# Optimization experiments

Hardware: AMD Instinct MI355X
Metric: run time of the kernel (lower is better)

## Reference

```python
import jax, jax.numpy as jnp
import numpy as np

B, C, H, W = 8, 256, 64, 64


def setup_inputs() -> dict:
    key = jax.random.key(0)
    ks = jax.random.split(key, 9)
    s = 1.0 / np.sqrt(C)  # conv2d default init scale
    return {
        "foreground": jax.random.normal(ks[0], (B, C, H, W), jnp.float32),
        "background": jax.random.normal(ks[1], (B, C, H, W), jnp.float32),
        "mask": jax.random.uniform(ks[2], (B, C, H, W), jnp.float32),
        "Wq": jax.random.normal(ks[3], (C, C), jnp.float32) * s,
        "bq": jnp.zeros((C,), jnp.float32),
        "Wk": jax.random.normal(ks[4], (C, C), jnp.float32) * s,
        "bk": jnp.zeros((C,), jnp.float32),
        "Wv": jax.random.normal(ks[5], (C, C), jnp.float32) * s,
        "bv": jnp.zeros((C,), jnp.float32),
        "gamma": jnp.ones((1,), jnp.float32),
    }


def _conv1x1(x, Wt, b):
    # 1x1 conv == per-pixel channel matmul; x: [B,C,H,W], Wt: [Cout,Cin]
    return jnp.einsum('bchw,oc->bohw', x, Wt) + b[None, :, None, None]


def reference(foreground, background, mask, Wq, bq, Wk, bk, Wv, bv, gamma):
    b, c, h, w = foreground.shape
    hw = h * w
    # mask is already at feature resolution (interpolate would be identity)
    q = _conv1x1(foreground, Wq, bq).reshape(b, c, hw)   # [B,C,HW]
    k = _conv1x1(background, Wk, bk).reshape(b, c, hw)   # [B,C,HW]
    # bmm(q, k^T): channel-channel correlation [B,C,C]
    corr = jnp.einsum('bci,bdi->bcd', q, k)
    m_r = mask.reshape(b, c, hw)                          # [B,C,HW]
    # bmm(corr, m_r): mask-modulated scores [B,C,HW]
    scores = jnp.einsum('bcd,bdi->bci', corr, m_r)
    energy = jax.nn.softmax(scores, axis=-1)
    v = _conv1x1(foreground, Wv, bv).reshape(b, c, hw)
    attended = (energy * v).reshape(b, c, h, w)
    out = foreground * mask + gamma[0] * (1.0 - mask) * attended
    return out
```

## Files before the change

### kernel.cpp

```cpp
#include <hip/hip_runtime.h>
#include <math.h>

#define B_    8
#define C_    256
#define HW_   4096
#define CHW_  ((long)C_ * HW_)

#define BKT   32
#define LDH   40
#define KS    16
#define KCH   (HW_ / KS)

typedef __attribute__((ext_vector_type(8))) short bf16x8;
typedef __attribute__((ext_vector_type(4))) float f32x4;
#define MFMA_BF16(a, b, c) __builtin_amdgcn_mfma_f32_16x16x32_bf16((a), (b), (c), 0, 0, 0)

union frag_u { uint4 u4; bf16x8 bf; };

__device__ __forceinline__ void cvt_hl4(const float4 f, uint* h, uint* l) {
    uint u0 = __float_as_uint(f.x), u1 = __float_as_uint(f.y),
         u2 = __float_as_uint(f.z), u3 = __float_as_uint(f.w);
    uint h0 = (u0 + 0x8000u) & 0xFFFF0000u, h1 = (u1 + 0x8000u) & 0xFFFF0000u,
         h2 = (u2 + 0x8000u) & 0xFFFF0000u, h3 = (u3 + 0x8000u) & 0xFFFF0000u;
    h[0] = (h0 >> 16) | h1;
    h[1] = (h2 >> 16) | h3;
    float l0 = f.x - __uint_as_float(h0), l1 = f.y - __uint_as_float(h1),
          l2 = f.z - __uint_as_float(h2), l3 = f.w - __uint_as_float(h3);
    uint a0 = __float_as_uint(l0) & 0xFFFF0000u, a1 = __float_as_uint(l1) & 0xFFFF0000u,
         a2 = __float_as_uint(l2) & 0xFFFF0000u, a3 = __float_as_uint(l3) & 0xFFFF0000u;
    l[0] = (a0 >> 16) | a1;
    l[1] = (a2 >> 16) | a3;
}
__device__ __forceinline__ void cvt_h4(const float4 f, uint* h) {
    uint u0 = __float_as_uint(f.x), u1 = __float_as_uint(f.y),
         u2 = __float_as_uint(f.z), u3 = __float_as_uint(f.w);
    uint h0 = (u0 + 0x8000u) & 0xFFFF0000u, h1 = (u1 + 0x8000u) & 0xFFFF0000u,
         h2 = (u2 + 0x8000u) & 0xFFFF0000u, h3 = (u3 + 0x8000u) & 0xFFFF0000u;
    h[0] = (h0 >> 16) | h1;
    h[1] = (h2 >> 16) | h3;
}

__device__ __forceinline__ void cvt2_hl(float a, float b2, uint* h, uint* l) {
    uint ua = __float_as_uint(a), ub = __float_as_uint(b2);
    uint ha = (ua + 0x8000u) & 0xFFFF0000u, hb = (ub + 0x8000u) & 0xFFFF0000u;
    *h = (ha >> 16) | hb;
    float la = a - __uint_as_float(ha), lb = b2 - __uint_as_float(hb);
    *l = ((__float_as_uint(la) & 0xFFFF0000u) >> 16) | (__float_as_uint(lb) & 0xFFFF0000u);
}
__device__ __forceinline__ uint cvt2_h(float a, float b2) {
    uint ha = (__float_as_uint(a) + 0x8000u) & 0xFFFF0000u;
    uint hb = (__float_as_uint(b2) + 0x8000u) & 0xFFFF0000u;
    return (ha >> 16) | hb;
}

__global__ __launch_bounds__(256) void conv_w(
    const float* __restrict__ Wv, ushort* __restrict__ Wvh)
{
    const int i = (blockIdx.x * 256 + threadIdx.x) * 4;
    float4 v = *reinterpret_cast<const float4*>(&Wv[i]);
    uint h[2];
    cvt_h4(v, h);
    *reinterpret_cast<uint2*>(&Wvh[i]) = make_uint2(h[0], h[1]);
}

__global__ __launch_bounds__(256) void transpose_cvt(
    const float* __restrict__ mask, const float* __restrict__ fg,
    ushort* __restrict__ mTh, ushort* __restrict__ mTl, ushort* __restrict__ fTh)
{
    __shared__ float Ms[64][65];
    __shared__ float Fs[64][65];

    const int b  = blockIdx.z;
    const int c0 = blockIdx.y * 64;
    const int i0 = blockIdx.x * 64;
    const int t  = threadIdx.x;

    const int lr = t >> 2;
    const int lc = (t & 3) * 16;
    const float* mp = mask + (long)b * CHW_ + (long)(c0 + lr) * HW_ + i0 + lc;
    const float* fp = fg   + (long)b * CHW_ + (long)(c0 + lr) * HW_ + i0 + lc;
    #pragma unroll
    for (int j = 0; j < 16; j += 4) {
        *reinterpret_cast<float4*>(&Ms[lr][lc + j]) = *reinterpret_cast<const float4*>(mp + j);
        *reinterpret_cast<float4*>(&Fs[lr][lc + j]) = *reinterpret_cast<const float4*>(fp + j);
    }
    __syncthreads();

    const int oi = t >> 2;
    const int oc = (t & 3) * 16;
    uint hm[8], lm[8], hf[8];
    #pragma unroll
    for (int j = 0; j < 8; ++j) {
        const float m0v = Ms[oc + 2 * j][oi], m1v = Ms[oc + 2 * j + 1][oi];
        cvt2_hl(m0v, m1v, &hm[j], &lm[j]);
        hf[j] = cvt2_h(Fs[oc + 2 * j][oi], Fs[oc + 2 * j + 1][oi]);
    }
    const long ro = ((long)b * HW_ + i0 + oi) * C_ + c0 + oc;
    *reinterpret_cast<uint4*>(&mTh[ro])     = make_uint4(hm[0], hm[1], hm[2], hm[3]);
    *reinterpret_cast<uint4*>(&mTh[ro + 8]) = make_uint4(hm[4], hm[5], hm[6], hm[7]);
    *reinterpret_cast<uint4*>(&mTl[ro])     = make_uint4(lm[0], lm[1], lm[2], lm[3]);
    *reinterpret_cast<uint4*>(&mTl[ro + 8]) = make_uint4(lm[4], lm[5], lm[6], lm[7]);
    *reinterpret_cast<uint4*>(&fTh[ro])     = make_uint4(hf[0], hf[1], hf[2], hf[3]);
    *reinterpret_cast<uint4*>(&fTh[ro + 8]) = make_uint4(hf[4], hf[5], hf[6], hf[7]);
}

__global__ __launch_bounds__(256, 3) void gemm_nt_mfma(
    const float* __restrict__ F, const float* __restrict__ G,
    float* __restrict__ part,
    float* __restrict__ fsum, float* __restrict__ gsum)
{
    __shared__ ushort Ah[128 * LDH], Al[128 * LDH], Bh[128 * LDH], Bl[128 * LDH];

    const int z  = blockIdx.z;
    const int b  = z >> 4;
    const int ks = z & (KS - 1);
    const int c0 = blockIdx.y * 128;
    const int d0 = blockIdx.x * 128;
    const float* Fb = F + (long)b * CHW_ + (long)ks * KCH;
    const float* Gb = G + (long)b * CHW_ + (long)ks * KCH;
    const bool doF = (blockIdx.x == 0);
    const bool doG = (blockIdx.y == 0);

    const int t    = threadIdx.x;
    const int srow = t & 127;
    const int skf  = (t >> 7) * 16;
    const int lane = t & 63, w = t >> 6;
    const int col  = lane & 15, quad = lane >> 4;
    const int wm   = (w >> 1) * 64, wn = (w & 1) * 64;

    f32x4 acc[4][4] = {};
    float rsF = 0.0f, rsG = 0.0f;

    for (int kt = 0; kt < KCH; kt += BKT) {
        {
            const float* s = &Fb[(long)(c0 + srow) * HW_ + kt + skf];
            float4 v0 = *reinterpret_cast<const float4*>(s);
            float4 v1 = *reinterpret_cast<const float4*>(s + 4);
            float4 v2 = *reinterpret_cast<const float4*>(s + 8);
            float4 v3 = *reinterpret_cast<const float4*>(s + 12);
            if (doF) {
                rsF += (v0.x + v0.y + v0.z + v0.w) + (v1.x + v1.y + v1.z + v1.w)
                     + (v2.x + v2.y + v2.z + v2.w) + (v3.x + v3.y + v3.z + v3.w);
            }
            uint h[4], l[4];
            cvt_hl4(v0, h + 0, l + 0);
            cvt_hl4(v1, h + 2, l + 2);
            *reinterpret_cast<uint4*>(&Ah[srow * LDH + skf]) = make_uint4(h[0], h[1], h[2], h[3]);
            *reinterpret_cast<uint4*>(&Al[srow * LDH + skf]) = make_uint4(l[0], l[1], l[2], l[3]);
            cvt_hl4(v2, h + 0, l + 0);
            cvt_hl4(v3, h + 2, l + 2);
            *reinterpret_cast<uint4*>(&Ah[srow * LDH + skf + 8]) = make_uint4(h[0], h[1], h[2], h[3]);
            *reinterpret_cast<uint4*>(&Al[srow * LDH + skf + 8]) = make_uint4(l[0], l[1], l[2], l[3]);
        }
        {
            const float* s = &Gb[(long)(d0 + srow) * HW_ + kt + skf];
            float4 v0 = *reinterpret_cast<const float4*>(s);
            float4 v1 = *reinterpret_cast<const float4*>(s + 4);
            float4 v2 = *reinterpret_cast<const float4*>(s + 8);
            float4 v3 = *reinterpret_cast<const float4*>(s + 12);
            if (doG) {
                rsG += (v0.x + v0.y + v0.z + v0.w) + (v1.x + v1.y + v1.z + v1.w)
                     + (v2.x + v2.y + v2.z + v2.w) + (v3.x + v3.y + v3.z + v3.w);
            }
            uint h[4], l[4];
            cvt_hl4(v0, h + 0, l + 0);
            cvt_hl4(v1, h + 2, l + 2);
            *reinterpret_cast<uint4*>(&Bh[srow * LDH + skf]) = make_uint4(h[0], h[1], h[2], h[3]);
            *reinterpret_cast<uint4*>(&Bl[srow * LDH + skf]) = make_uint4(l[0], l[1], l[2], l[3]);
            cvt_hl4(v2, h + 0, l + 0);
            cvt_hl4(v3, h + 2, l + 2);
            *reinterpret_cast<uint4*>(&Bh[srow * LDH + skf + 8]) = make_uint4(h[0], h[1], h[2], h[3]);
            *reinterpret_cast<uint4*>(&Bl[srow * LDH + skf + 8]) = make_uint4(l[0], l[1], l[2], l[3]);
        }
        __syncthreads();

        bf16x8 bfh[4], bfl[4];
        #pragma unroll
        for (int tj = 0; tj < 4; ++tj) {
            const int r = (wn + tj * 16 + col) * LDH + quad * 8;
            bfh[tj] = *reinterpret_cast<const bf16x8*>(&Bh[r]);
            bfl[tj] = *reinterpret_cast<const bf16x8*>(&Bl[r]);
        }
        #pragma unroll
        for (int ti = 0; ti < 4; ++ti) {
            const int r = (wm + ti * 16 + col) * LDH + quad * 8;
            bf16x8 afh = *reinterpret_cast<const bf16x8*>(&Ah[r]);
            bf16x8 afl = *reinterpret_cast<const bf16x8*>(&Al[r]);
            #pragma unroll
            for (int tj = 0; tj < 4; ++tj) {
                acc[ti][tj] = MFMA_BF16(afh, bfh[tj], acc[ti][tj]);
                acc[ti][tj] = MFMA_BF16(afh, bfl[tj], acc[ti][tj]);
                acc[ti][tj] = MFMA_BF16(afl, bfh[tj], acc[ti][tj]);
            }
        }
        __syncthreads();
    }

    if (doF) atomicAdd(&fsum[b * C_ + c0 + srow], rsF);
    if (doG) atomicAdd(&gsum[b * C_ + d0 + srow], rsG);

    float* P = part + (long)z * C_ * C_;
    #pragma unroll
    for (int ti = 0; ti < 4; ++ti) {
        const int m = c0 + wm + ti * 16 + quad * 4;
        #pragma unroll
        for (int tj = 0; tj < 4; ++tj) {
            const int n = d0 + wn + tj * 16 + col;
            #pragma unroll
            for (int r = 0; r < 4; ++r)
                P[(long)(m + r) * C_ + n] = acc[ti][tj][r];
        }
    }
}

__global__ __launch_bounds__(256, 2) void gemm_stats_mfma(
    const ushort* __restrict__ corrh, const ushort* __restrict__ corrl,
    const ushort* __restrict__ mTh,   const ushort* __restrict__ mTl,
    float* __restrict__ pmax, float* __restrict__ psum)
{
    __shared__ float pm[2][128], ps[2][128];

    const int b  = blockIdx.z;
    const int m0 = blockIdx.y * 128;
    const int n0 = blockIdx.x * 128;
    const ushort* Ahb = corrh + (long)b * C_ * C_;
    const ushort* Alb = corrl + (long)b * C_ * C_;
    const ushort* Bhb = mTh + (long)b * HW_ * C_;
    const ushort* Blb = mTl + (long)b * HW_ * C_;

    const int t    = threadIdx.x;
    const int lane = t & 63, w = t >> 6;
    const int col  = lane & 15, quad = lane >> 4;
    const int wm   = (w >> 1) * 64, wn = (w & 1) * 64;

    f32x4 acc[4][4] = {};

    #pragma unroll 1
    for (int kt = 0; kt < C_; kt += BKT) {
        bf16x8 ah[4], al[4], bh[4], bl[4];
        #pragma unroll
        for (int ti = 0; ti < 4; ++ti) {
            const long oa = (long)(m0 + wm + ti * 16 + col) * C_ + kt + quad * 8;
            ah[ti] = *reinterpret_cast<const bf16x8*>(&Ahb[oa]);
            al[ti] = *reinterpret_cast<const bf16x8*>(&Alb[oa]);
        }
        #pragma unroll
        for (int tj = 0; tj < 4; ++tj) {
            const long ob = (long)(n0 + wn + tj * 16 + col) * C_ + kt + quad * 8;
            bh[tj] = *reinterpret_cast<const bf16x8*>(&Bhb[ob]);
            bl[tj] = *reinterpret_cast<const bf16x8*>(&Blb[ob]);
        }
        #pragma unroll
        for (int tj = 0; tj < 4; ++tj) {
            #pragma unroll
            for (int ti = 0; ti < 4; ++ti) {
                acc[ti][tj] = MFMA_BF16(ah[ti], bh[tj], acc[ti][tj]);
                acc[ti][tj] = MFMA_BF16(ah[ti], bl[tj], acc[ti][tj]);
                acc[ti][tj] = MFMA_BF16(al[ti], bh[tj], acc[ti][tj]);
            }
        }
    }

    #pragma unroll
    for (int ti = 0; ti < 4; ++ti) {
        #pragma unroll
        for (int r = 0; r < 4; ++r) {
            float mx = fmaxf(fmaxf(acc[ti][0][r], acc[ti][1][r]),
                             fmaxf(acc[ti][2][r], acc[ti][3][r]));
            mx = fmaxf(mx, __shfl_xor(mx, 1));
            mx = fmaxf(mx, __shfl_xor(mx, 2));
            mx = fmaxf(mx, __shfl_xor(mx, 4));
            mx = fmaxf(mx, __shfl_xor(mx, 8));
            float se2 = __expf(acc[ti][0][r] - mx) + __expf(acc[ti][1][r] - mx)
                      + __expf(acc[ti][2][r] - mx) + __expf(acc[ti][3][r] - mx);
            se2 += __shfl_xor(se2, 1);
            se2 += __shfl_xor(se2, 2);
            se2 += __shfl_xor(se2, 4);
            se2 += __shfl_xor(se2, 8);
            if (col == 0) {
                const int rb = wm + ti * 16 + quad * 4 + r;
                pm[w & 1][rb] = mx;
                ps[w & 1][rb] = se2;
            }
        }
    }
    __syncthreads();
    if (t < 128) {
        const float a0 = pm[0][t], a1 = pm[1][t];
        const float gm = fmaxf(a0, a1);
        const float gs = ps[0][t] * __expf(a0 - gm) + ps[1][t] * __expf(a1 - gm);
        const long rowg = (long)b * C_ + m0 + t;
        pmax[rowg * 32 + blockIdx.x] = gm;
        psum[rowg * 32 + blockIdx.x] = gs;
    }
}

__global__ __launch_bounds__(256, 2) void gemm_fused_final(
    const ushort* __restrict__ corrh, const ushort* __restrict__ corrl,
    const ushort* __restrict__ Wvh,
    const ushort* __restrict__ mTh,   const ushort* __restrict__ mTl,
    const ushort* __restrict__ fTh,
    const float* __restrict__ mask,   const float* __restrict__ fg,
    const float* __restrict__ pmax,   const float* __restrict__ psum,
    const float* __restrict__ bv,     const float* __restrict__ gamma,
    float* __restrict__ out)
{
    __shared__ float sm[128], si[128];

    const int b  = blockIdx.z;
    const int m0 = blockIdx.y * 128;
    const int n0 = blockIdx.x * 128;
    const ushort* Ahb = corrh + (long)b * C_ * C_;
    const ushort* Alb = corrl + (long)b * C_ * C_;
    const ushort* Bhb = mTh + (long)b * HW_ * C_;
    const ushort* Blb = mTl + (long)b * HW_ * C_;
    const ushort* Bfb = fTh + (long)b * HW_ * C_;

    const int t    = threadIdx.x;
    const int lane = t & 63, w = t >> 6;
    const int col  = lane & 15, quad = lane >> 4;
    const int wm   = (w >> 1) * 64, wn = (w & 1) * 64;

    if (t < 128) {
        const long rowg = (long)b * C_ + m0 + t;
        const float* pmr = pmax + rowg * 32;
        const float* psr = psum + rowg * 32;
        float gm = -INFINITY;
        #pragma unroll
        for (int i = 0; i < 32; ++i) gm = fmaxf(gm, pmr[i]);
        float gs = 0.0f;
        #pragma unroll
        for (int i = 0; i < 32; ++i) gs += psr[i] * __expf(pmr[i] - gm);
        sm[t] = gm;
        si[t] = 1.0f / gs;
    }

    f32x4 acc_s[4][4] = {};
    f32x4 acc_v[4][4] = {};

    #pragma unroll 1
    for (int kt = 0; kt < C_; kt += BKT) {
        bf16x8 ah[4], al[4], aw[4], bh[4], bl[4], bf[4];
        #pragma unroll
        for (int ti = 0; ti < 4; ++ti) {
            const long oa = (long)(m0 + wm + ti * 16 + col) * C_ + kt + quad * 8;
            ah[ti] = *reinterpret_cast<const bf16x8*>(&Ahb[oa]);
            al[ti] = *reinterpret_cast<const bf16x8*>(&Alb[oa]);
            aw[ti] = *reinterpret_cast<const bf16x8*>(&Wvh[oa]);
        }
        #pragma unroll
        for (int tj = 0; tj < 4; ++tj) {
            const long ob = (long)(n0 + wn + tj * 16 + col) * C_ + kt + quad * 8;
            bh[tj] = *reinterpret_cast<const bf16x8*>(&Bhb[ob]);
            bl[tj] = *reinterpret_cast<const bf16x8*>(&Blb[ob]);
            bf[tj] = *reinterpret_cast<const bf16x8*>(&Bfb[ob]);
        }
        #pragma unroll
        for (int tj = 0; tj < 4; ++tj) {
            #pragma unroll
            for (int ti = 0; ti < 4; ++ti) {
                acc_s[ti][tj] = MFMA_BF16(ah[ti], bh[tj], acc_s[ti][tj]);
                acc_s[ti][tj] = MFMA_BF16(ah[ti], bl[tj], acc_s[ti][tj]);
                acc_s[ti][tj] = MFMA_BF16(al[ti], bh[tj], acc_s[ti][tj]);
                acc_v[ti][tj] = MFMA_BF16(aw[ti], bf[tj], acc_v[ti][tj]);
            }
        }
    }

    __syncthreads();

    const float g = gamma[0];
    #pragma unroll
    for (int ti = 0; ti < 4; ++ti) {
        #pragma unroll
        for (int r = 0; r < 4; ++r) {
            const int lrow = wm + ti * 16 + quad * 4 + r;
            const float mx  = sm[lrow];
            const float inv = si[lrow] * g;
            #pragma unroll
            for (int tj = 0; tj < 4; ++tj)
                acc_s[ti][tj][r] = __expf(acc_s[ti][tj][r] - mx) * inv;
        }
    }

    #pragma unroll
    for (int ti = 0; ti < 4; ++ti) {
        const int m = m0 + wm + ti * 16 + quad * 4;
        #pragma unroll
        for (int r = 0; r < 4; ++r) {
            const float bvm = bv[m + r];
            #pragma unroll
            for (int tj = 0; tj < 4; ++tj) {
                const int n = n0 + wn + tj * 16 + col;
                const long e = (long)b * CHW_ + (long)(m + r) * HW_ + n;
                const float f  = fg[e];
                const float mk = mask[e];
                const float vv = acc_v[ti][tj][r] + bvm;
                out[e] = f * mk + (1.0f - mk) * acc_s[ti][tj][r] * vv;
            }
        }
    }
}

__global__ __launch_bounds__(256) void reduce_part(
    const float* __restrict__ part, float* __restrict__ S1)
{
    const long idx = (long)blockIdx.x * 256 + threadIdx.x;
    const int  b   = (int)(idx >> 16);
    const long e   = idx & 65535;
    const float* p = part + ((long)b * KS) * 65536 + e;
    float s = 0.0f;
    #pragma unroll
    for (int ks = 0; ks < KS; ++ks) s += p[(long)ks * 65536];
    S1[idx] = s;
}

#define BK64 16
#define LDT64 68
__global__ __launch_bounds__(256) void gemm_nt64(
    const float* __restrict__ S1, const float* __restrict__ Wk,
    float* __restrict__ T)
{
    __shared__ float As[BK64][LDT64];
    __shared__ float Bs[BK64][LDT64];
    const int r0 = blockIdx.y * 64;
    const int d0 = blockIdx.x * 64;
    const int t   = threadIdx.x;
    const int tx  = t & 15, ty = t >> 4;
    const int tx4 = tx * 4, ty4 = ty * 4;
    const int am  = t >> 2, ak4 = (t & 3) * 4;

    float acc[4][4] = {};
    for (int k0 = 0; k0 < C_; k0 += BK64) {
        float4 av = *reinterpret_cast<const float4*>(&S1[(long)(r0 + am) * C_ + k0 + ak4]);
        float4 bw = *reinterpret_cast<const float4*>(&Wk[(long)(d0 + am) * C_ + k0 + ak4]);
        As[ak4+0][am]=av.x; As[ak4+1][am]=av.y; As[ak4+2][am]=av.z; As[ak4+3][am]=av.w;
        Bs[ak4+0][am]=bw.x; Bs[ak4+1][am]=bw.y; Bs[ak4+2][am]=bw.z; Bs[ak4+3][am]=bw.w;
        __syncthreads();
        #pragma unroll
        for (int kk = 0; kk < BK64; ++kk) {
            float4 a = *reinterpret_cast<const float4*>(&As[kk][ty4]);
            float4 x = *reinterpret_cast<const float4*>(&Bs[kk][tx4]);
            const float ar[4] = {a.x,a.y,a.z,a.w};
            const float xr[4] = {x.x,x.y,x.z,x.w};
            #pragma unroll
            for (int r = 0; r < 4; ++r)
                #pragma unroll
                for (int s = 0; s < 4; ++s)
                    acc[r][s] = fmaf(ar[r], xr[s], acc[r][s]);
        }
        __syncthreads();
    }
    #pragma unroll
    for (int r = 0; r < 4; ++r) {
        float4 o; o.x=acc[r][0]; o.y=acc[r][1]; o.z=acc[r][2]; o.w=acc[r][3];
        *reinterpret_cast<float4*>(&T[(long)(r0 + ty4 + r) * C_ + d0 + tx4]) = o;
    }
}

__global__ __launch_bounds__(256) void gemm_nn64_rank1(
    const float* __restrict__ Wq, const float* __restrict__ T,
    const float* __restrict__ Wk, const float* __restrict__ bk,
    const float* __restrict__ bq,
    const float* __restrict__ fsum, const float* __restrict__ gsum,
    ushort* __restrict__ corrh, ushort* __restrict__ corrl)
{
    __shared__ float As[BK64][LDT64];
    __shared__ float Bs[BK64][LDT64];
    __shared__ float u_s[64], wh_s[64];
    const int b  = blockIdx.z;
    const int m0 = blockIdx.y * 64;
    const int n0 = blockIdx.x * 64;
    const float* Tb = T + (long)b * C_ * C_;

    const int t   = threadIdx.x;
    const int tx  = t & 15, ty = t >> 4;
    const int tx4 = tx * 4, ty4 = ty * 4;
    const int am  = t >> 2, ak4 = (t & 3) * 4;
    const int xk  = ty,     xn4 = tx4;

    if (t < 64) {
        const float* wrow = Wq + (long)(m0 + t) * C_;
        const float* s = fsum + b * C_;
        float a = 0.0f;
        for (int e2 = 0; e2 < C_; ++e2) a = fmaf(wrow[e2], s[e2], a);
        u_s[t] = a;
    } else if (t < 128) {
        const int d = n0 + (t - 64);
        const float* wrow = Wk + (long)d * C_;
        const float* s = gsum + b * C_;
        float a = 0.0f;
        for (int e2 = 0; e2 < C_; ++e2) a = fmaf(wrow[e2], s[e2], a);
        wh_s[t - 64] = a + (float)HW_ * bk[d];
    }

    float acc[4][4] = {};
    for (int k0 = 0; k0 < C_; k0 += BK64) {
        float4 av = *reinterpret_cast<const float4*>(&Wq[(long)(m0 + am) * C_ + k0 + ak4]);
        float4 xv = *reinterpret_cast<const float4*>(&Tb[(long)(k0 + xk) * C_ + n0 + xn4]);
        As[ak4+0][am]=av.x; As[ak4+1][am]=av.y; As[ak4+2][am]=av.z; As[ak4+3][am]=av.w;
        *reinterpret_cast<float4*>(&Bs[xk][xn4]) = xv;
        __syncthreads();
        #pragma unroll
        for (int kk = 0; kk < BK64; ++kk) {
            float4 a = *reinterpret_cast<const float4*>(&As[kk][ty4]);
            float4 x = *reinterpret_cast<const float4*>(&Bs[kk][tx4]);
            const float ar[4] = {a.x,a.y,a.z,a.w};
            const float xr[4] = {x.x,x.y,x.z,x.w};
            #pragma unroll
            for (int r = 0; r < 4; ++r)
                #pragma unroll
                for (int s = 0; s < 4; ++s)
                    acc[r][s] = fmaf(ar[r], xr[s], acc[r][s]);
        }
        __syncthreads();
    }

    float4 bkv = *reinterpret_cast<const float4*>(&bk[n0 + tx4]);
    float4 whv = make_float4(wh_s[tx4], wh_s[tx4+1], wh_s[tx4+2], wh_s[tx4+3]);
    #pragma unroll
    for (int r = 0; r < 4; ++r) {
        const int m = m0 + ty4 + r;
        const float um = u_s[ty4 + r];
        const float bm = bq[m];
        float4 o;
        o.x = acc[r][0] + um*bkv.x + bm*whv.x;
        o.y = acc[r][1] + um*bkv.y + bm*whv.y;
        o.z = acc[r][2] + um*bkv.z + bm*whv.z;
        o.w = acc[r][3] + um*bkv.w + bm*whv.w;
        uint h[2], l[2];
        cvt_hl4(o, h, l);
        const long e = (long)b * C_ * C_ + (long)m * C_ + n0 + tx4;
        *reinterpret_cast<uint2*>(&corrh[e]) = make_uint2(h[0], h[1]);
        *reinterpret_cast<uint2*>(&corrl[e]) = make_uint2(l[0], l[1]);
    }
}

extern "C" void kernel_launch(void* const* d_in, const int* in_sizes, int n_in,
                              void* d_out, int out_size, void* d_ws, size_t ws_size,
                              hipStream_t stream)
{
    const float* fg    = (const float*)d_in[0];
    const float* bg    = (const float*)d_in[1];
    const float* mask  = (const float*)d_in[2];
    const float* Wq    = (const float*)d_in[3];
    const float* bq    = (const float*)d_in[4];
    const float* Wk    = (const float*)d_in[5];
    const float* bk    = (const float*)d_in[6];
    const float* Wv    = (const float*)d_in[7];
    const float* bv    = (const float*)d_in[8];
    const float* gamma = (const float*)d_in[9];
    float* out = (float*)d_out;

    char* ws = (char*)d_ws;
    float*  part   = (float*)(ws);
    float*  S1     = (float*)(ws + 33554432);
    float*  T      = (float*)(ws + 35651584);
    ushort* corrh  = (ushort*)(ws + 37748736);
    ushort* corrl  = (ushort*)(ws + 38797312);
    ushort* Wvh    = (ushort*)(ws + 39845888);
    float*  fsum   = (float*)(ws + 39976960);
    float*  gsum   = (float*)(ws + 39985152);
    float*  pmax   = (float*)(ws + 39993344);
    float*  psum   = (float*)(ws + 40255488);
    ushort* mTh    = (ushort*)(ws);
    ushort* mTl    = (ushort*)(ws + 16777216);
    ushort* fTh    = (ushort*)(ws + 40517632);

    const dim3 blk(256);

    hipMemsetAsync(fsum, 0, 16384, stream);

    conv_w<<<dim3(64), blk, 0, stream>>>(Wv, Wvh);

    gemm_nt_mfma<<<dim3(2, 2, B_ * KS), blk, 0, stream>>>(fg, bg, part, fsum, gsum);
    reduce_part<<<dim3(B_ * C_ * C_ / 256), blk, 0, stream>>>(part, S1);

    transpose_cvt<<<dim3(HW_ / 64, C_ / 64, B_), blk, 0, stream>>>(
        mask, fg, mTh, mTl, fTh);

    gemm_nt64<<<dim3(C_ / 64, B_ * C_ / 64), blk, 0, stream>>>(S1, Wk, T);
    gemm_nn64_rank1<<<dim3(4, 4, B_), blk, 0, stream>>>(
        Wq, T, Wk, bk, bq, fsum, gsum, corrh, corrl);

    gemm_stats_mfma<<<dim3(HW_ / 128, C_ / 128, B_), blk, 0, stream>>>(
        corrh, corrl, mTh, mTl, pmax, psum);

    gemm_fused_final<<<dim3(HW_ / 128, C_ / 128, B_), blk, 0, stream>>>(
        corrh, corrl, Wvh, mTh, mTl, fTh, mask, fg, pmax, psum, bv, gamma, out);
}
```

Measured before the change: 324.7 us.

## Double-buffer B operand tiles in LDS via async global_load_lds in both GEMMs

In the two mask GEMM kernels, the B-operand tiles (mask transpose hi/lo and the foreground bf16 tile) are now staged into shared memory with async global-to-LDS loads. The LDS layout is XOR-swizzled and double-buffered so the next k-chunk loads while the current one feeds MFMA. This is meant to cut redundant global reads, since B was previously loaded per wave and both M-waves read the same rows, and to hide load latency. The cost is more LDS use, a barrier every k-step, and a change of launch bounds to 3 blocks per CU for the stats kernel, which may add register pressure.

```diff
diff --git a/kernel.cpp b/kernel.cpp
--- a/kernel.cpp
+++ b/kernel.cpp
@@ -10,12 +10,18 @@
 #define LDH   40
 #define KS    16
 #define KCH   (HW_ / KS)
+#define NCH   (C_ / BKT)
 
 typedef __attribute__((ext_vector_type(8))) short bf16x8;
 typedef __attribute__((ext_vector_type(4))) float f32x4;
 #define MFMA_BF16(a, b, c) __builtin_amdgcn_mfma_f32_16x16x32_bf16((a), (b), (c), 0, 0, 0)
 
 union frag_u { uint4 u4; bf16x8 bf; };
+
+#define GLOAD_LDS16(src, dst)                                              \
+    __builtin_amdgcn_global_load_lds(                                      \
+        (const __attribute__((address_space(1))) void*)(src),              \
+        (__attribute__((address_space(3))) void*)(dst), 16, 0, 0)
 
 __device__ __forceinline__ void cvt_hl4(const float4 f, uint* h, uint* l) {
     uint u0 = __float_as_uint(f.x), u1 = __float_as_uint(f.y),
@@ -213,11 +219,12 @@
     }
 }
 
-__global__ __launch_bounds__(256, 2) void gemm_stats_mfma(
+__global__ __launch_bounds__(256, 3) void gemm_stats_mfma(
     const ushort* __restrict__ corrh, const ushort* __restrict__ corrl,
     const ushort* __restrict__ mTh,   const ushort* __restrict__ mTl,
     float* __restrict__ pmax, float* __restrict__ psum)
 {
+    __shared__ __align__(16) ushort Bst[2][2][4096];
     __shared__ float pm[2][128], ps[2][128];
 
     const int b  = blockIdx.z;
@@ -232,24 +239,59 @@
     const int lane = t & 63, w = t >> 6;
     const int col  = lane & 15, quad = lane >> 4;
     const int wm   = (w >> 1) * 64, wn = (w & 1) * 64;
+    const int qsw  = (lane & 3) ^ ((lane >> 3) & 3);
+    const int srw  = lane >> 2;
+
+    const ushort* gsrcs[2] = { Bhb, Blb };
+
+#define STAGE_S(buf, kk) do {                                              \
+    _Pragma("unroll")                                                      \
+    for (int a = 0; a < 2; ++a) {                                          \
+        _Pragma("unroll")                                                  \
+        for (int gg = 0; gg < 2; ++gg) {                                   \
+            const int g = w * 2 + gg;                                      \
+            const ushort* src = gsrcs[a]                                   \
+                + (long)(n0 + g * 16 + srw) * C_ + (kk) + qsw * 8;         \
+            GLOAD_LDS16(src, &Bst[buf][a][g * 512]);                       \
+        }                                                                  \
+    }                                                                      \
+} while (0)
+
+    int boff[4];
+    #pragma unroll
+    for (int tj = 0; tj < 4; ++tj) {
+        const int rowB = wn + tj * 16 + col;
+        boff[tj] = rowB * 64 + ((quad ^ ((rowB >> 1) & 3)) << 4);
+    }
 
     f32x4 acc[4][4] = {};
 
+    STAGE_S(0, 0);
+    __syncthreads();
+
+    int cur = 0;
     #pragma unroll 1
-    for (int kt = 0; kt < C_; kt += BKT) {
-        bf16x8 ah[4], al[4], bh[4], bl[4];
+    for (int kc = 0; kc < NCH; ++kc) {
+        const int kt = kc * BKT;
+
+        bf16x8 ah[4], al[4];
         #pragma unroll
         for (int ti = 0; ti < 4; ++ti) {
             const long oa = (long)(m0 + wm + ti * 16 + col) * C_ + kt + quad * 8;
             ah[ti] = *reinterpret_cast<const bf16x8*>(&Ahb[oa]);
             al[ti] = *reinterpret_cast<const bf16x8*>(&Alb[oa]);
         }
+
+        if (kc + 1 < NCH) STAGE_S(cur ^ 1, kt + BKT);
+
+        const char* base = (const char*)&Bst[cur][0][0];
+        bf16x8 bh[4], bl[4];
         #pragma unroll
         for (int tj = 0; tj < 4; ++tj) {
-            const long ob = (long)(n0 + wn + tj * 16 + col) * C_ + kt + quad * 8;
-            bh[tj] = *reinterpret_cast<const bf16x8*>(&Bhb[ob]);
-            bl[tj] = *reinterpret_cast<const bf16x8*>(&Blb[ob]);
-        }
+            bh[tj] = *reinterpret_cast<const bf16x8*>(base + boff[tj]);
+            bl[tj] = *reinterpret_cast<const bf16x8*>(base + 8192 + boff[tj]);
+        }
+
         #pragma unroll
         for (int tj = 0; tj < 4; ++tj) {
             #pragma unroll
@@ -259,7 +301,10 @@
                 acc[ti][tj] = MFMA_BF16(al[ti], bh[tj], acc[ti][tj]);
             }
         }
-    }
+        __syncthreads();
+        cur ^= 1;
+    }
+#undef STAGE_S
 
     #pragma unroll
     for (int ti = 0; ti < 4; ++ti) {
@@ -305,6 +350,7 @@
     const float* __restrict__ bv,     const float* __restrict__ gamma,
     float* __restrict__ out)
 {
+    __shared__ __align__(16) ushort Bst[2][3][4096];
     __shared__ float sm[128], si[128];
 
     const int b  = blockIdx.z;
@@ -320,6 +366,23 @@
     const int lane = t & 63, w = t >> 6;
     const int col  = lane & 15, quad = lane >> 4;
     const int wm   = (w >> 1) * 64, wn = (w & 1) * 64;
+    const int qsw  = (lane & 3) ^ ((lane >> 3) & 3);
+    const int srw  = lane >> 2;
+
+    const ushort* gsrcs[3] = { Bhb, Blb, Bfb };
+
+#define STAGE_F(buf, kk) do {                                              \
+    _Pragma("unroll")                                                      \
+    for (int a = 0; a < 3; ++a) {                                          \
+        _Pragma("unroll")                                                  \
+        for (int gg = 0; gg < 2; ++gg) {                                   \
+            const int g = w * 2 + gg;                                      \
+            const ushort* src = gsrcs[a]                                   \
+                + (long)(n0 + g * 16 + srw) * C_ + (kk) + qsw * 8;         \
+            GLOAD_LDS16(src, &Bst[buf][a][g * 512]);                       \
+        }                                                                  \
+    }                                                                      \
+} while (0)
 
     if (t < 128) {
         const long rowg = (long)b * C_ + m0 + t;
@@ -335,12 +398,25 @@
         si[t] = 1.0f / gs;
     }
 
+    int boff[4];
+    #pragma unroll
+    for (int tj = 0; tj < 4; ++tj) {
+        const int rowB = wn + tj * 16 + col;
+        boff[tj] = rowB * 64 + ((quad ^ ((rowB >> 1) & 3)) << 4);
+    }
+
     f32x4 acc_s[4][4] = {};
     f32x4 acc_v[4][4] = {};
 
+    STAGE_F(0, 0);
+    __syncthreads();
+
+    int cur = 0;
     #pragma unroll 1
-    for (int kt = 0; kt < C_; kt += BKT) {
-        bf16x8 ah[4], al[4], aw[4], bh[4], bl[4], bf[4];
+    for (int kc = 0; kc < NCH; ++kc) {
+        const int kt = kc * BKT;
+
+        bf16x8 ah[4], al[4], aw[4];
         #pragma unroll
         for (int ti = 0; ti < 4; ++ti) {
             const long oa = (long)(m0 + wm + ti * 16 + col) * C_ + kt + quad * 8;
@@ -348,13 +424,18 @@
             al[ti] = *reinterpret_cast<const bf16x8*>(&Alb[oa]);
             aw[ti] = *reinterpret_cast<const bf16x8*>(&Wvh[oa]);
         }
+
+        if (kc + 1 < NCH) STAGE_F(cur ^ 1, kt + BKT);
+
+        const char* base = (const char*)&Bst[cur][0][0];
+        bf16x8 bh[4], bl[4], bf[4];
         #pragma unroll
         for (int tj = 0; tj < 4; ++tj) {
-            const long ob = (long)(n0 + wn + tj * 16 + col) * C_ + kt + quad * 8;
-            bh[tj] = *reinterpret_cast<const bf16x8*>(&Bhb[ob]);
-            bl[tj] = *reinterpret_cast<const bf16x8*>(&Blb[ob]);
-            bf[tj] = *reinterpret_cast<const bf16x8*>(&Bfb[ob]);
-        }
+            bh[tj] = *reinterpret_cast<const bf16x8*>(base + boff[tj]);
+            bl[tj] = *reinterpret_cast<const bf16x8*>(base + 8192 + boff[tj]);
+            bf[tj] = *reinterpret_cast<const bf16x8*>(base + 16384 + boff[tj]);
+        }
+
         #pragma unroll
         for (int tj = 0; tj < 4; ++tj) {
             #pragma unroll
@@ -365,9 +446,10 @@
                 acc_v[ti][tj] = MFMA_BF16(aw[ti], bf[tj], acc_v[ti][tj]);
             }
         }
-    }
-
-    __syncthreads();
+        __syncthreads();
+        cur ^= 1;
+    }
+#undef STAGE_F
 
     const float g = gamma[0];
     #pragma unroll
```

After: 297.8 us. 1.09x faster.

## Stage MFMA operands through swizzled LDS via global_load_lds and coalesce stores

Applied to the files above, without the earlier changes.

The stats and fused-final GEMMs now stream their bf16 operand tiles into XOR-swizzled shared memory with direct global-to-LDS loads, instead of having each wave issue its own strided global vector loads. Occupancy hints go from 2 to 3 blocks. The split-K partial GEMM stages its output through LDS so it can write coalesced float4 rows, and reduce_part is vectorised to float4. The partial-max/sum buffers move to the S1 region and are read with float4 loads. In exchange this adds barrier overhead per K chunk, has no double buffering, and relies on the aliased workspace regions not overlapping any live data.

```diff
diff --git a/kernel.cpp b/kernel.cpp
--- a/kernel.cpp
+++ b/kernel.cpp
@@ -10,12 +10,19 @@
 #define LDH   40
 #define KS    16
 #define KCH   (HW_ / KS)
+#define NCH   (C_ / BKT)
+#define NPB   32
 
 typedef __attribute__((ext_vector_type(8))) short bf16x8;
 typedef __attribute__((ext_vector_type(4))) float f32x4;
 #define MFMA_BF16(a, b, c) __builtin_amdgcn_mfma_f32_16x16x32_bf16((a), (b), (c), 0, 0, 0)
 
 union frag_u { uint4 u4; bf16x8 bf; };
+
+#define GLOAD_LDS16(src, dst)                                              \
+    __builtin_amdgcn_global_load_lds(                                      \
+        (const __attribute__((address_space(1))) void*)(src),              \
+        (__attribute__((address_space(3))) void*)(dst), 16, 0, 0)
 
 __device__ __forceinline__ void cvt_hl4(const float4 f, uint* h, uint* l) {
     uint u0 = __float_as_uint(f.x), u1 = __float_as_uint(f.y),
@@ -109,7 +116,9 @@
     float* __restrict__ part,
     float* __restrict__ fsum, float* __restrict__ gsum)
 {
-    __shared__ ushort Ah[128 * LDH], Al[128 * LDH], Bh[128 * LDH], Bl[128 * LDH];
+    __shared__ __align__(16) ushort SMEM[4][128 * LDH];
+    ushort* Ah = SMEM[0]; ushort* Al = SMEM[1];
+    ushort* Bh = SMEM[2]; ushort* Bl = SMEM[3];
 
     const int z  = blockIdx.z;
     const int b  = z >> 4;
@@ -199,25 +208,38 @@
     if (doF) atomicAdd(&fsum[b * C_ + c0 + srow], rsF);
     if (doG) atomicAdd(&gsum[b * C_ + d0 + srow], rsG);
 
+    float* xch = (float*)&SMEM[0][0];
     float* P = part + (long)z * C_ * C_;
+    const int pr = t >> 3, pu = t & 7;
+    const int mmb = c0 + ((pr & 16) ? 64 : 0) + (pr & 15);
     #pragma unroll
     for (int ti = 0; ti < 4; ++ti) {
-        const int m = c0 + wm + ti * 16 + quad * 4;
+        __syncthreads();
         #pragma unroll
         for (int tj = 0; tj < 4; ++tj) {
-            const int n = d0 + wn + tj * 16 + col;
-            #pragma unroll
-            for (int r = 0; r < 4; ++r)
-                P[(long)(m + r) * C_ + n] = acc[ti][tj][r];
-        }
-    }
-}
-
-__global__ __launch_bounds__(256, 2) void gemm_stats_mfma(
+            const int lc = wn + tj * 16 + col;
+            #pragma unroll
+            for (int r = 0; r < 4; ++r) {
+                const int lr = (w >> 1) * 16 + quad * 4 + r;
+                xch[lr * 132 + lc] = acc[ti][tj][r];
+            }
+        }
+        __syncthreads();
+        const int mm = mmb + ti * 16;
+        float* dst = &P[(long)mm * C_ + d0 + pu * 16];
+        const float* srcx = &xch[pr * 132 + pu * 16];
+        #pragma unroll
+        for (int j = 0; j < 16; j += 4)
+            *reinterpret_cast<float4*>(dst + j) = *reinterpret_cast<const float4*>(srcx + j);
+    }
+}
+
+__global__ __launch_bounds__(256, 3) void gemm_stats_mfma(
     const ushort* __restrict__ corrh, const ushort* __restrict__ corrl,
     const ushort* __restrict__ mTh,   const ushort* __restrict__ mTl,
     float* __restrict__ pmax, float* __restrict__ psum)
 {
+    __shared__ __align__(16) ushort S_[4][4096];
     __shared__ float pm[2][128], ps[2][128];
 
     const int b  = blockIdx.z;
@@ -232,23 +254,41 @@
     const int lane = t & 63, w = t >> 6;
     const int col  = lane & 15, quad = lane >> 4;
     const int wm   = (w >> 1) * 64, wn = (w & 1) * 64;
+    const int qsw  = (lane & 3) ^ ((lane >> 3) & 3);
+    const int srw  = lane >> 2;
+
+    int aoff[4], boff[4];
+    #pragma unroll
+    for (int tt = 0; tt < 4; ++tt) {
+        const int rowA = wm + tt * 16 + col;
+        aoff[tt] = rowA * 64 + ((quad ^ ((rowA >> 1) & 3)) << 4);
+        const int rowB = wn + tt * 16 + col;
+        boff[tt] = rowB * 64 + ((quad ^ ((rowB >> 1) & 3)) << 4);
+    }
 
     f32x4 acc[4][4] = {};
 
     #pragma unroll 1
-    for (int kt = 0; kt < C_; kt += BKT) {
+    for (int kc = 0; kc < NCH; ++kc) {
+        const int kt = kc * BKT;
+        #pragma unroll
+        for (int gg = 0; gg < 2; ++gg) {
+            const int rbase = w * 32 + gg * 16;
+            const long rsrc = rbase + srw;
+            GLOAD_LDS16(Ahb + (long)(m0 + rsrc) * C_ + kt + qsw * 8, &S_[0][rbase * 32]);
+            GLOAD_LDS16(Alb + (long)(m0 + rsrc) * C_ + kt + qsw * 8, &S_[1][rbase * 32]);
+            GLOAD_LDS16(Bhb + (long)(n0 + rsrc) * C_ + kt + qsw * 8, &S_[2][rbase * 32]);
+            GLOAD_LDS16(Blb + (long)(n0 + rsrc) * C_ + kt + qsw * 8, &S_[3][rbase * 32]);
+        }
+        __syncthreads();
+
         bf16x8 ah[4], al[4], bh[4], bl[4];
         #pragma unroll
-        for (int ti = 0; ti < 4; ++ti) {
-            const long oa = (long)(m0 + wm + ti * 16 + col) * C_ + kt + quad * 8;
-            ah[ti] = *reinterpret_cast<const bf16x8*>(&Ahb[oa]);
-            al[ti] = *reinterpret_cast<const bf16x8*>(&Alb[oa]);
-        }
-        #pragma unroll
-        for (int tj = 0; tj < 4; ++tj) {
-            const long ob = (long)(n0 + wn + tj * 16 + col) * C_ + kt + quad * 8;
-            bh[tj] = *reinterpret_cast<const bf16x8*>(&Bhb[ob]);
-            bl[tj] = *reinterpret_cast<const bf16x8*>(&Blb[ob]);
+        for (int tt = 0; tt < 4; ++tt) {
+            ah[tt] = *reinterpret_cast<const bf16x8*>((const char*)&S_[0][0] + aoff[tt]);
+            al[tt] = *reinterpret_cast<const bf16x8*>((const char*)&S_[1][0] + aoff[tt]);
+            bh[tt] = *reinterpret_cast<const bf16x8*>((const char*)&S_[2][0] + boff[tt]);
+            bl[tt] = *reinterpret_cast<const bf16x8*>((const char*)&S_[3][0] + boff[tt]);
         }
         #pragma unroll
         for (int tj = 0; tj < 4; ++tj) {
@@ -259,6 +299,7 @@
                 acc[ti][tj] = MFMA_BF16(al[ti], bh[tj], acc[ti][tj]);
             }
         }
+        __syncthreads();
     }
 
     #pragma unroll
@@ -290,12 +331,12 @@
         const float gm = fmaxf(a0, a1);
         const float gs = ps[0][t] * __expf(a0 - gm) + ps[1][t] * __expf(a1 - gm);
         const long rowg = (long)b * C_ + m0 + t;
-        pmax[rowg * 32 + blockIdx.x] = gm;
-        psum[rowg * 32 + blockIdx.x] = gs;
-    }
-}
-
-__global__ __launch_bounds__(256, 2) void gemm_fused_final(
+        pmax[rowg * NPB + blockIdx.x] = gm;
+        psum[rowg * NPB + blockIdx.x] = gs;
+    }
+}
+
+__global__ __launch_bounds__(256, 3) void gemm_fused_final(
     const ushort* __restrict__ corrh, const ushort* __restrict__ corrl,
     const ushort* __restrict__ Wvh,
     const ushort* __restrict__ mTh,   const ushort* __restrict__ mTl,
@@ -305,6 +346,7 @@
     const float* __restrict__ bv,     const float* __restrict__ gamma,
     float* __restrict__ out)
 {
+    __shared__ __align__(16) ushort S_[6][4096];
     __shared__ float sm[128], si[128];
 
     const int b  = blockIdx.z;
@@ -320,40 +362,74 @@
     const int lane = t & 63, w = t >> 6;
     const int col  = lane & 15, quad = lane >> 4;
     const int wm   = (w >> 1) * 64, wn = (w & 1) * 64;
-
-    if (t < 128) {
-        const long rowg = (long)b * C_ + m0 + t;
-        const float* pmr = pmax + rowg * 32;
-        const float* psr = psum + rowg * 32;
+    const int qsw  = (lane & 3) ^ ((lane >> 3) & 3);
+    const int srw  = lane >> 2;
+
+    {
+        const int row  = t >> 1;
+        const int part = t & 1;
+        const long rowg = (long)b * C_ + m0 + row;
+        const float* pmr = pmax + rowg * NPB + part * 16;
+        const float* psr = psum + rowg * NPB + part * 16;
+        float4 pv[4], sv[4];
+        #pragma unroll
+        for (int j = 0; j < 4; ++j) {
+            pv[j] = *reinterpret_cast<const float4*>(pmr + j * 4);
+            sv[j] = *reinterpret_cast<const float4*>(psr + j * 4);
+        }
         float gm = -INFINITY;
         #pragma unroll
-        for (int i = 0; i < 32; ++i) gm = fmaxf(gm, pmr[i]);
+        for (int j = 0; j < 4; ++j)
+            gm = fmaxf(gm, fmaxf(fmaxf(pv[j].x, pv[j].y), fmaxf(pv[j].z, pv[j].w)));
+        gm = fmaxf(gm, __shfl_xor(gm, 1));
         float gs = 0.0f;
         #pragma unroll
-        for (int i = 0; i < 32; ++i) gs += psr[i] * __expf(pmr[i] - gm);
-        sm[t] = gm;
-        si[t] = 1.0f / gs;
+        for (int j = 0; j < 4; ++j) {
+            gs += sv[j].x * __expf(pv[j].x - gm) + sv[j].y * __expf(pv[j].y - gm)
+                + sv[j].z * __expf(pv[j].z - gm) + sv[j].w * __expf(pv[j].w - gm);
+        }
+        gs += __shfl_xor(gs, 1);
+        sm[row] = gm;
+        si[row] = 1.0f / gs;
+    }
+
+    int aoff[4], boff[4];
+    #pragma unroll
+    for (int tt = 0; tt < 4; ++tt) {
+        const int rowA = wm + tt * 16 + col;
+        aoff[tt] = rowA * 64 + ((quad ^ ((rowA >> 1) & 3)) << 4);
+        const int rowB = wn + tt * 16 + col;
+        boff[tt] = rowB * 64 + ((quad ^ ((rowB >> 1) & 3)) << 4);
     }
 
     f32x4 acc_s[4][4] = {};
     f32x4 acc_v[4][4] = {};
 
     #pragma unroll 1
-    for (int kt = 0; kt < C_; kt += BKT) {
+    for (int kc = 0; kc < NCH; ++kc) {
+        const int kt = kc * BKT;
+        #pragma unroll
+        for (int gg = 0; gg < 2; ++gg) {
+            const int rbase = w * 32 + gg * 16;
+            const long rsrc = rbase + srw;
+            GLOAD_LDS16(Ahb + (long)(m0 + rsrc) * C_ + kt + qsw * 8, &S_[0][rbase * 32]);
+            GLOAD_LDS16(Alb + (long)(m0 + rsrc) * C_ + kt + qsw * 8, &S_[1][rbase * 32]);
+            GLOAD_LDS16(Wvh + (long)(m0 + rsrc) * C_ + kt + qsw * 8, &S_[2][rbase * 32]);
+            GLOAD_LDS16(Bhb + (long)(n0 + rsrc) * C_ + kt + qsw * 8, &S_[3][rbase * 32]);
+            GLOAD_LDS16(Blb + (long)(n0 + rsrc) * C_ + kt + qsw * 8, &S_[4][rbase * 32]);
+            GLOAD_LDS16(Bfb + (long)(n0 + rsrc) * C_ + kt + qsw * 8, &S_[5][rbase * 32]);
+        }
+        __syncthreads();
+
         bf16x8 ah[4], al[4], aw[4], bh[4], bl[4], bf[4];
         #pragma unroll
-        for (int ti = 0; ti < 4; ++ti) {
-            const long oa = (long)(m0 + wm + ti * 16 + col) * C_ + kt + quad * 8;
-            ah[ti] = *reinterpret_cast<const bf16x8*>(&Ahb[oa]);
-            al[ti] = *reinterpret_cast<const bf16x8*>(&Alb[oa]);
-            aw[ti] = *reinterpret_cast<const bf16x8*>(&Wvh[oa]);
-        }
-        #pragma unroll
-        for (int tj = 0; tj < 4; ++tj) {
-            const long ob = (long)(n0 + wn + tj * 16 + col) * C_ + kt + quad * 8;
-            bh[tj] = *reinterpret_cast<const bf16x8*>(&Bhb[ob]);
-            bl[tj] = *reinterpret_cast<const bf16x8*>(&Blb[ob]);
-            bf[tj] = *reinterpret_cast<const bf16x8*>(&Bfb[ob]);
+        for (int tt = 0; tt < 4; ++tt) {
+            ah[tt] = *reinterpret_cast<const bf16x8*>((const char*)&S_[0][0] + aoff[tt]);
+            al[tt] = *reinterpret_cast<const bf16x8*>((const char*)&S_[1][0] + aoff[tt]);
+            aw[tt] = *reinterpret_cast<const bf16x8*>((const char*)&S_[2][0] + aoff[tt]);
+            bh[tt] = *reinterpret_cast<const bf16x8*>((const char*)&S_[3][0] + boff[tt]);
+            bl[tt] = *reinterpret_cast<const bf16x8*>((const char*)&S_[4][0] + boff[tt]);
+            bf[tt] = *reinterpret_cast<const bf16x8*>((const char*)&S_[5][0] + boff[tt]);
         }
         #pragma unroll
         for (int tj = 0; tj < 4; ++tj) {
@@ -365,9 +441,8 @@
                 acc_v[ti][tj] = MFMA_BF16(aw[ti], bf[tj], acc_v[ti][tj]);
             }
         }
-    }
-
-    __syncthreads();
+        __syncthreads();
+    }
 
     const float g = gamma[0];
     #pragma unroll
@@ -405,14 +480,17 @@
 __global__ __launch_bounds__(256) void reduce_part(
     const float* __restrict__ part, float* __restrict__ S1)
 {
-    const long idx = (long)blockIdx.x * 256 + threadIdx.x;
-    const int  b   = (int)(idx >> 16);
-    const long e   = idx & 65535;
+    const long i4 = ((long)blockIdx.x * 256 + threadIdx.x) * 4;
+    const int  b  = (int)(i4 >> 16);
+    const long e  = i4 & 65535;
     const float* p = part + ((long)b * KS) * 65536 + e;
-    float s = 0.0f;
-    #pragma unroll
-    for (int ks = 0; ks < KS; ++ks) s += p[(long)ks * 65536];
-    S1[idx] = s;
+    float4 s = make_float4(0.f, 0.f, 0.f, 0.f);
+    #pragma unroll
+    for (int ks = 0; ks < KS; ++ks) {
+        float4 v = *reinterpret_cast<const float4*>(&p[(long)ks * 65536]);
+        s.x += v.x; s.y += v.y; s.z += v.z; s.w += v.w;
+    }
+    *reinterpret_cast<float4*>(&S1[i4]) = s;
 }
 
 #define BK64 16
@@ -561,8 +639,8 @@
     ushort* Wvh    = (ushort*)(ws + 39845888);
     float*  fsum   = (float*)(ws + 39976960);
     float*  gsum   = (float*)(ws + 39985152);
-    float*  pmax   = (float*)(ws + 39993344);
-    float*  psum   = (float*)(ws + 40255488);
+    float*  pmax   = (float*)(ws + 33554432);
+    float*  psum   = (float*)(ws + 33816576);
     ushort* mTh    = (ushort*)(ws);
     ushort* mTl    = (ushort*)(ws + 16777216);
     ushort* fTh    = (ushort*)(ws + 40517632);
@@ -574,7 +652,7 @@
     conv_w<<<dim3(64), blk, 0, stream>>>(Wv, Wvh);
 
     gemm_nt_mfma<<<dim3(2, 2, B_ * KS), blk, 0, stream>>>(fg, bg, part, fsum, gsum);
-    reduce_part<<<dim3(B_ * C_ * C_ / 256), blk, 0, stream>>>(part, S1);
+    reduce_part<<<dim3(B_ * C_ * C_ / 1024), blk, 0, stream>>>(part, S1);
 
     transpose_cvt<<<dim3(HW_ / 64, C_ / 64, B_), blk, 0, stream>>>(
         mask, fg, mTh, mTl, fTh);
```

Result: faster. 309.0 us (-4.8%).
